# Performance work log

Measured on AMD Instinct MI355X. Metric: run time of the kernel, lower is better.

## Reference

```python
import jax, jax.numpy as jnp
import numpy as np

N = 50000      # nodes
E = 800000     # edges (before self loops)
IN, H, OUT = 128, 64, 64
NEG_SLOPE = 0.2  # PyG GATConv leaky_relu slope


def _glorot(k, shape):
    lim = float(np.sqrt(6.0 / (shape[0] + shape[1])))
    return jax.random.uniform(k, shape, jnp.float32, -lim, lim)


def setup_inputs() -> dict:
    key = jax.random.key(0)
    ks = jax.random.split(key, 16)
    x = jax.random.normal(ks[0], (N, IN), jnp.float32)
    edge_src = jax.random.randint(ks[1], (E,), 0, N, jnp.int32)
    edge_dst = jax.random.randint(ks[2], (E,), 0, N, jnp.int32)
    dims = [(IN, H), (H, H), (H, OUT)]
    inp = {"x": x, "edge_src": edge_src, "edge_dst": edge_dst}
    i = 3
    for l, (di, do) in enumerate(dims):
        inp[f"W{l}"] = _glorot(ks[i], (di, do)); i += 1
        inp[f"as{l}"] = _glorot(ks[i], (1, do))[0]; i += 1
        inp[f"ad{l}"] = _glorot(ks[i], (1, do))[0]; i += 1
        inp[f"b{l}"] = jnp.zeros((do,), jnp.float32)
    return inp


def _gat_layer(x, W, a_src, a_dst, b, src, dst):
    # single-head GATConv (PyG semantics, self loops already in src/dst)
    h = x @ W                              # [N, do]
    s = h @ a_src                          # [N] source attention logits
    d = h @ a_dst                          # [N] dest attention logits
    e = jax.nn.leaky_relu(s[src] + d[dst], NEG_SLOPE)   # [E']
    # segment softmax over incoming edges of each destination node
    m = jax.ops.segment_max(e, dst, num_segments=N)
    w = jnp.exp(e - m[dst])
    denom = jax.ops.segment_sum(w, dst, num_segments=N)
    coef = w / (denom[dst] + 1e-16)
    out = jax.ops.segment_sum(h[src] * coef[:, None], dst, num_segments=N)
    return out + b


def reference(x, edge_src, edge_dst, W0, as0, ad0, b0, W1, as1, ad1, b1, W2, as2, ad2, b2):
    # add self loops (GATConv default add_self_loops=True)
    loop = jnp.arange(N, dtype=edge_src.dtype)
    src = jnp.concatenate([edge_src, loop])
    dst = jnp.concatenate([edge_dst, loop])
    h = jax.nn.relu(_gat_layer(x, W0, as0, ad0, b0, src, dst))
    # dropout is identity in eval mode
    h = jax.nn.relu(_gat_layer(h, W1, as1, ad1, b1, src, dst))
    return _gat_layer(h, W2, as2, ad2, b2, src, dst)
```

## Files before the change

### kernel.cpp

```cpp
#include <hip/hip_runtime.h>
#include <hip/hip_fp16.h>
#include <math.h>

#define WAVE 64
#define NEG_SLOPE 0.2f
#define LSTR 68


__global__ __launch_bounds__(256) void bucket_count_kernel(
    const int* __restrict__ dst, int* __restrict__ gcnt, int e, int nb) {
    extern __shared__ int cnt[];
    for (int b = threadIdx.x; b < nb; b += 256) cnt[b] = 0;
    __syncthreads();
    int base = blockIdx.x * 4096;
#pragma unroll
    for (int k = 0; k < 16; ++k) {
        int i = base + k * 256 + threadIdx.x;
        if (i < e) atomicAdd(&cnt[dst[i] >> 7], 1);
    }
    __syncthreads();
    for (int b = threadIdx.x; b < nb; b += 256) {
        int c = cnt[b];
        if (c) atomicAdd(&gcnt[b], c);
    }
}

__global__ __launch_bounds__(512) void bucket_scan_kernel(
    const int* __restrict__ gcnt, int* __restrict__ boff, int* __restrict__ gfill,
    int* __restrict__ rowptr, int nb, int e, int n) {
    __shared__ int sh[512];
    int t = threadIdx.x;
    int v = (t < nb) ? gcnt[t] : 0;
    sh[t] = v;
    __syncthreads();
    for (int o = 1; o < 512; o <<= 1) {
        int u = (t >= o) ? sh[t - o] : 0;
        __syncthreads();
        sh[t] += u;
        __syncthreads();
    }
    if (t < nb) { int ex = sh[t] - v; boff[t] = ex; gfill[t] = ex; }
    if (t == 0) { boff[nb] = e; rowptr[n] = e + n; }
}

__global__ __launch_bounds__(256) void bucket_place_kernel(
    const int* __restrict__ src, const int* __restrict__ dst,
    int* __restrict__ gfill, int2* __restrict__ binned, int e, int nb) {
    extern __shared__ int lds[];
    int* cnt = lds;
    int* bas = lds + nb;
    for (int b = threadIdx.x; b < nb; b += 256) cnt[b] = 0;
    __syncthreads();
    int base = blockIdx.x * 4096;
#pragma unroll
    for (int k = 0; k < 16; ++k) {
        int i = base + k * 256 + threadIdx.x;
        if (i < e) atomicAdd(&cnt[dst[i] >> 7], 1);
    }
    __syncthreads();
    for (int b = threadIdx.x; b < nb; b += 256) {
        int c = cnt[b];
        bas[b] = c ? atomicAdd(&gfill[b], c) : 0;
        cnt[b] = 0;
    }
    __syncthreads();
#pragma unroll
    for (int k = 0; k < 16; ++k) {
        int i = base + k * 256 + threadIdx.x;
        if (i < e) {
            int d = dst[i];
            int bk = d >> 7;
            int r = atomicAdd(&cnt[bk], 1);
            binned[bas[bk] + r] = make_int2(src[i], d);
        }
    }
}

__global__ __launch_bounds__(256) void bucket_build_kernel(
    const int2* __restrict__ binned, const int* __restrict__ boff,
    int* __restrict__ csr_src, int* __restrict__ rowptr, int n) {
    __shared__ int cnt[128], off[128], pcnt[128];
    int b = blockIdx.x;
    int t = threadIdx.x;
    int nodeBase = b << 7;
    int nc = min(128, n - nodeBase);
    int e0 = boff[b], e1 = boff[b + 1];
    int ne = e1 - e0;
    if (t < 128) { cnt[t] = 1; pcnt[t] = 1; }
    __syncthreads();
    for (int i = t; i < ne; i += 256)
        atomicAdd(&cnt[binned[e0 + i].y - nodeBase], 1);
    __syncthreads();
    if (t < 128) off[t] = cnt[t];
    __syncthreads();
    for (int o = 1; o < 128; o <<= 1) {
        int u = (t >= o && t < 128) ? off[t - o] : 0;
        __syncthreads();
        if (t < 128) off[t] += u;
        __syncthreads();
    }
    if (t < 128) off[t] -= cnt[t];
    __syncthreads();
    int csrBase = e0 + nodeBase;
    if (t < nc) {
        rowptr[nodeBase + t] = csrBase + off[t];
        csr_src[csrBase + off[t]] = nodeBase + t;
    }
    for (int i = t; i < ne; i += 256) {
        int2 p = binned[e0 + i];
        int loc = p.y - nodeBase;
        int r = atomicAdd(&pcnt[loc], 1);
        csr_src[csrBase + off[loc] + r] = p.x;
    }
}


template <int K>
__global__ __launch_bounds__(256) void gemm_feat_kernel(
    const float* __restrict__ X, const float* __restrict__ W,
    const float* __restrict__ a_s, const float* __restrict__ a_d,
    __half* __restrict__ H, float* __restrict__ S, float* __restrict__ D, int n) {
    __shared__ float Xs[64 * LSTR];
    __shared__ float Ws[64 * LSTR];
    int t = threadIdx.x;
    int tx = t & 15;
    int ty = t >> 4;
    int base = blockIdx.x * 64;
    float acc[4][4] = {};

    int q = t & 3;
    int srow = t >> 2;

    for (int k0 = 0; k0 < K; k0 += 64) {
        int grow = base + srow;
#pragma unroll
        for (int j = 0; j < 4; ++j) {
            int c = 16 * j + 4 * q;
            float4 v = make_float4(0.f, 0.f, 0.f, 0.f);
            if (grow < n) v = *(const float4*)(X + (size_t)grow * K + k0 + c);
            *(float4*)(Xs + srow * LSTR + c) = v;
            float4 w = *(const float4*)(W + (size_t)(k0 + srow) * 64 + c);
            *(float4*)(Ws + srow * LSTR + c) = w;
        }
        __syncthreads();
#pragma unroll 8
        for (int kk = 0; kk < 64; ++kk) {
            float4 wv = *(const float4*)(Ws + kk * LSTR + 4 * tx);
#pragma unroll
            for (int i = 0; i < 4; ++i) {
                float xv = Xs[(4 * ty + i) * LSTR + kk];
                acc[i][0] = fmaf(xv, wv.x, acc[i][0]);
                acc[i][1] = fmaf(xv, wv.y, acc[i][1]);
                acc[i][2] = fmaf(xv, wv.z, acc[i][2]);
                acc[i][3] = fmaf(xv, wv.w, acc[i][3]);
            }
        }
        __syncthreads();
    }

    const float4 av_s = *(const float4*)(a_s + 4 * tx);
    const float4 av_d = *(const float4*)(a_d + 4 * tx);
#pragma unroll
    for (int i = 0; i < 4; ++i) {
        int row = base + 4 * ty + i;
        bool ok = row < n;
        if (ok) {
            __half2 h01 = __floats2half2_rn(acc[i][0], acc[i][1]);
            __half2 h23 = __floats2half2_rn(acc[i][2], acc[i][3]);
            uint2 u;
            u.x = *(unsigned int*)&h01;
            u.y = *(unsigned int*)&h23;
            *(uint2*)(H + (size_t)row * 64 + 4 * tx) = u;
        }
        float ps = acc[i][0] * av_s.x + acc[i][1] * av_s.y +
                   acc[i][2] * av_s.z + acc[i][3] * av_s.w;
        float pd = acc[i][0] * av_d.x + acc[i][1] * av_d.y +
                   acc[i][2] * av_d.z + acc[i][3] * av_d.w;
        for (int o = 1; o < 16; o <<= 1) {
            ps += __shfl_xor(ps, o);
            pd += __shfl_xor(pd, o);
        }
        if (tx == 0 && ok) { S[row] = ps; D[row] = pd; }
    }
}


__global__ __launch_bounds__(256) void gat_aggregate_kernel(
    const __half* __restrict__ H, const float* __restrict__ S,
    const float* __restrict__ D, const int* __restrict__ rowptr,
    const int* __restrict__ csr_src, const float* __restrict__ bias,
    float* __restrict__ OUT, int n, int do_relu) {
    int wid  = (blockIdx.x * blockDim.x + threadIdx.x) >> 6;
    int lane = threadIdx.x & 63;
    if (wid >= n) return;
    int eg = lane >> 4;
    int cg = lane & 15;
    int start = rowptr[wid];
    int end   = rowptr[wid + 1];
    float d_i = D[wid];

    float z = 0.f;
    float4 acc = make_float4(0.f, 0.f, 0.f, 0.f);

    for (int cb = start; cb < end; cb += WAVE) {
        int j = cb + lane;
        bool v = j < end;
        int sc = v ? csr_src[j] : 0;
        float sv = S[sc];
        float e = sv + d_i;
        e = (e > 0.f) ? e : NEG_SLOPE * e;
        float w = v ? __expf(e) : 0.f;

        int nch = min(WAVE, end - cb);
        int rounds = (nch + 3) >> 2;
#pragma unroll 4
        for (int r = 0; r < rounds; ++r) {
            int idx = 4 * r + eg;
            float wr = __shfl(w, idx);
            int   sr = __shfl(sc, idx);
            float2 f0 = make_float2(0.f, 0.f), f1 = f0;
            if (idx < nch) {
                uint2 u = *(const uint2*)(H + (size_t)sr * 64 + 4 * cg);
                f0 = __half22float2(*(__half2*)&u.x);
                f1 = __half22float2(*(__half2*)&u.y);
            }
            z += wr;
            acc.x = fmaf(wr, f0.x, acc.x);
            acc.y = fmaf(wr, f0.y, acc.y);
            acc.z = fmaf(wr, f1.x, acc.z);
            acc.w = fmaf(wr, f1.y, acc.w);
        }
    }

    for (int o = 16; o < 64; o <<= 1) {
        acc.x += __shfl_xor(acc.x, o);
        acc.y += __shfl_xor(acc.y, o);
        acc.z += __shfl_xor(acc.z, o);
        acc.w += __shfl_xor(acc.w, o);
        z     += __shfl_xor(z, o);
    }

    if (eg == 0) {
        float inv = 1.f / (z + 1e-16f);
        const float4 bv = *(const float4*)(bias + 4 * cg);
        float4 o4;
        o4.x = acc.x * inv + bv.x;
        o4.y = acc.y * inv + bv.y;
        o4.z = acc.z * inv + bv.z;
        o4.w = acc.w * inv + bv.w;
        if (do_relu) {
            o4.x = fmaxf(o4.x, 0.f); o4.y = fmaxf(o4.y, 0.f);
            o4.z = fmaxf(o4.z, 0.f); o4.w = fmaxf(o4.w, 0.f);
        }
        *(float4*)(OUT + (size_t)wid * 64 + 4 * cg) = o4;
    }
}


static inline size_t align256(size_t x) { return (x + 255) & ~(size_t)255; }

extern "C" void kernel_launch(void* const* d_in, const int* in_sizes, int n_in,
                              void* d_out, int out_size, void* d_ws, size_t ws_size,
                              hipStream_t stream) {
    const float* x    = (const float*)d_in[0];
    const int*   esrc = (const int*)d_in[1];
    const int*   edst = (const int*)d_in[2];
    const int E = in_sizes[1];
    const int N = in_sizes[0] / 128;

    const float* W0 = (const float*)d_in[3];
    const float* as0 = (const float*)d_in[4];
    const float* ad0 = (const float*)d_in[5];
    const float* b0 = (const float*)d_in[6];
    const float* W1 = (const float*)d_in[7];
    const float* as1 = (const float*)d_in[8];
    const float* ad1 = (const float*)d_in[9];
    const float* b1 = (const float*)d_in[10];
    const float* W2 = (const float*)d_in[11];
    const float* as2 = (const float*)d_in[12];
    const float* ad2 = (const float*)d_in[13];
    const float* b2 = (const float*)d_in[14];

    const int NB = (N + 127) >> 7;

    char* p = (char*)d_ws;
    int* gcnt    = (int*)p; p += align256((size_t)(NB + 1) * 4);
    int* boff    = (int*)p; p += align256((size_t)(NB + 1) * 4);
    int* gfill   = (int*)p; p += align256((size_t)(NB + 1) * 4);
    int* rowptr  = (int*)p; p += align256((size_t)(N + 1) * 4);
    int* csr_src = (int*)p; p += align256((size_t)(E + N) * 4);
    int2* binned = (int2*)p; p += align256((size_t)E * 8);
    __half* h16 = (__half*)p; p += align256((size_t)N * 64 * 2);
    float* sA = (float*)p; p += align256((size_t)N * 4);
    float* dA = (float*)p; p += align256((size_t)N * 4);
    float* XA = (float*)p; p += align256((size_t)N * 64 * 4);
    float* XB = (float*)p; p += align256((size_t)N * 64 * 4);
    float* out = (float*)d_out;

    int nchunk = (E + 4095) / 4096;
    hipMemsetAsync(gcnt, 0, (size_t)(NB + 1) * 4, stream);
    bucket_count_kernel<<<nchunk, 256, NB * 4, stream>>>(edst, gcnt, E, NB);
    bucket_scan_kernel<<<1, 512, 0, stream>>>(gcnt, boff, gfill, rowptr, NB, E, N);
    bucket_place_kernel<<<nchunk, 256, 2 * NB * 4, stream>>>(esrc, edst, gfill, binned, E, NB);
    bucket_build_kernel<<<NB, 256, 0, stream>>>(binned, boff, csr_src, rowptr, N);

    int tile_grid = (N + 63) / 64;
    int agg_grid  = (N + 3) / 4;

    gemm_feat_kernel<128><<<tile_grid, 256, 0, stream>>>(x, W0, as0, ad0, h16, sA, dA, N);
    gat_aggregate_kernel<<<agg_grid, 256, 0, stream>>>(h16, sA, dA, rowptr, csr_src, b0, XA, N, 1);

    gemm_feat_kernel<64><<<tile_grid, 256, 0, stream>>>(XA, W1, as1, ad1, h16, sA, dA, N);
    gat_aggregate_kernel<<<agg_grid, 256, 0, stream>>>(h16, sA, dA, rowptr, csr_src, b1, XB, N, 1);

    gemm_feat_kernel<64><<<tile_grid, 256, 0, stream>>>(XB, W2, as2, ad2, h16, sA, dA, N);
    gat_aggregate_kernel<<<agg_grid, 256, 0, stream>>>(h16, sA, dA, rowptr, csr_src, b2, out, N, 0);
}
```

Measured before the change: 272.3 us.

## Fuse aggregation with next-layer GEMM and merge edge counting into layer-0 GEMM

Layer-0 GEMM blocks and edge-count blocks now share one launch, with per-chunk partial counts written to memory instead of global atomics. A column scan in the scan kernel assigns deterministic per-chunk offsets, which removes the memset and the gfill atomics. Aggregation for layers 0 and 1 is fused with the following layer's feature GEMM in 1024-thread blocks, so the fp32 intermediate activations never go to global memory. The cost is a serial per-bucket loop over chunks in the single-block scan, and lower parallelism in the fused kernel, which reads W from global memory rather than LDS.

```diff
diff --git a/kernel.cpp b/kernel.cpp
--- a/kernel.cpp
+++ b/kernel.cpp
@@ -5,129 +5,39 @@
 #define WAVE 64
 #define NEG_SLOPE 0.2f
 #define LSTR 68
-
-
-__global__ __launch_bounds__(256) void bucket_count_kernel(
-    const int* __restrict__ dst, int* __restrict__ gcnt, int e, int nb) {
-    extern __shared__ int cnt[];
-    for (int b = threadIdx.x; b < nb; b += 256) cnt[b] = 0;
-    __syncthreads();
-    int base = blockIdx.x * 4096;
-#pragma unroll
-    for (int k = 0; k < 16; ++k) {
-        int i = base + k * 256 + threadIdx.x;
-        if (i < e) atomicAdd(&cnt[dst[i] >> 7], 1);
-    }
-    __syncthreads();
-    for (int b = threadIdx.x; b < nb; b += 256) {
-        int c = cnt[b];
-        if (c) atomicAdd(&gcnt[b], c);
-    }
-}
-
-__global__ __launch_bounds__(512) void bucket_scan_kernel(
-    const int* __restrict__ gcnt, int* __restrict__ boff, int* __restrict__ gfill,
-    int* __restrict__ rowptr, int nb, int e, int n) {
-    __shared__ int sh[512];
-    int t = threadIdx.x;
-    int v = (t < nb) ? gcnt[t] : 0;
-    sh[t] = v;
-    __syncthreads();
-    for (int o = 1; o < 512; o <<= 1) {
-        int u = (t >= o) ? sh[t - o] : 0;
-        __syncthreads();
-        sh[t] += u;
-        __syncthreads();
-    }
-    if (t < nb) { int ex = sh[t] - v; boff[t] = ex; gfill[t] = ex; }
-    if (t == 0) { boff[nb] = e; rowptr[n] = e + n; }
-}
-
-__global__ __launch_bounds__(256) void bucket_place_kernel(
-    const int* __restrict__ src, const int* __restrict__ dst,
-    int* __restrict__ gfill, int2* __restrict__ binned, int e, int nb) {
-    extern __shared__ int lds[];
-    int* cnt = lds;
-    int* bas = lds + nb;
-    for (int b = threadIdx.x; b < nb; b += 256) cnt[b] = 0;
-    __syncthreads();
-    int base = blockIdx.x * 4096;
-#pragma unroll
-    for (int k = 0; k < 16; ++k) {
-        int i = base + k * 256 + threadIdx.x;
-        if (i < e) atomicAdd(&cnt[dst[i] >> 7], 1);
-    }
-    __syncthreads();
-    for (int b = threadIdx.x; b < nb; b += 256) {
-        int c = cnt[b];
-        bas[b] = c ? atomicAdd(&gfill[b], c) : 0;
-        cnt[b] = 0;
-    }
-    __syncthreads();
-#pragma unroll
-    for (int k = 0; k < 16; ++k) {
-        int i = base + k * 256 + threadIdx.x;
-        if (i < e) {
-            int d = dst[i];
-            int bk = d >> 7;
-            int r = atomicAdd(&cnt[bk], 1);
-            binned[bas[bk] + r] = make_int2(src[i], d);
-        }
-    }
-}
-
-__global__ __launch_bounds__(256) void bucket_build_kernel(
-    const int2* __restrict__ binned, const int* __restrict__ boff,
-    int* __restrict__ csr_src, int* __restrict__ rowptr, int n) {
-    __shared__ int cnt[128], off[128], pcnt[128];
-    int b = blockIdx.x;
-    int t = threadIdx.x;
-    int nodeBase = b << 7;
-    int nc = min(128, n - nodeBase);
-    int e0 = boff[b], e1 = boff[b + 1];
-    int ne = e1 - e0;
-    if (t < 128) { cnt[t] = 1; pcnt[t] = 1; }
-    __syncthreads();
-    for (int i = t; i < ne; i += 256)
-        atomicAdd(&cnt[binned[e0 + i].y - nodeBase], 1);
-    __syncthreads();
-    if (t < 128) off[t] = cnt[t];
-    __syncthreads();
-    for (int o = 1; o < 128; o <<= 1) {
-        int u = (t >= o && t < 128) ? off[t - o] : 0;
-        __syncthreads();
-        if (t < 128) off[t] += u;
-        __syncthreads();
-    }
-    if (t < 128) off[t] -= cnt[t];
-    __syncthreads();
-    int csrBase = e0 + nodeBase;
-    if (t < nc) {
-        rowptr[nodeBase + t] = csrBase + off[t];
-        csr_src[csrBase + off[t]] = nodeBase + t;
-    }
-    for (int i = t; i < ne; i += 256) {
-        int2 p = binned[e0 + i];
-        int loc = p.y - nodeBase;
-        int r = atomicAdd(&pcnt[loc], 1);
-        csr_src[csrBase + off[loc] + r] = p.x;
-    }
-}
-
-
-template <int K>
-__global__ __launch_bounds__(256) void gemm_feat_kernel(
+#define CHUNK 8192
+
+
+__global__ __launch_bounds__(256) void count_gemm0_kernel(
+    const int* __restrict__ dst, int* __restrict__ part, int e, int nb, int nchunk,
     const float* __restrict__ X, const float* __restrict__ W,
     const float* __restrict__ a_s, const float* __restrict__ a_d,
     __half* __restrict__ H, float* __restrict__ S, float* __restrict__ D, int n) {
     __shared__ float Xs[64 * LSTR];
     __shared__ float Ws[64 * LSTR];
     int t = threadIdx.x;
+
+    if (blockIdx.x < nchunk) {
+        int* cnt = (int*)Ws;
+        for (int b = t; b < nb; b += 256) cnt[b] = 0;
+        __syncthreads();
+        int base = blockIdx.x * CHUNK;
+#pragma unroll
+        for (int k = 0; k < CHUNK / 256; ++k) {
+            int i = base + k * 256 + t;
+            if (i < e) atomicAdd(&cnt[dst[i] >> 7], 1);
+        }
+        __syncthreads();
+        for (int b = t; b < nb; b += 256)
+            part[(size_t)blockIdx.x * nb + b] = cnt[b];
+        return;
+    }
+
+    constexpr int K = 128;
     int tx = t & 15;
     int ty = t >> 4;
-    int base = blockIdx.x * 64;
+    int base = (blockIdx.x - nchunk) * 64;
     float acc[4][4] = {};
-
     int q = t & 3;
     int srow = t >> 2;
 
@@ -184,15 +94,111 @@
     }
 }
 
-
-__global__ __launch_bounds__(256) void gat_aggregate_kernel(
+__global__ __launch_bounds__(512) void bucket_scan_kernel(
+    int* __restrict__ part, int* __restrict__ boff, int* __restrict__ rowptr,
+    int nchunk, int nb, int e, int n) {
+    __shared__ int sh[512];
+    int t = threadIdx.x;
+    int total = 0;
+    if (t < nb) {
+        int run = 0;
+        for (int c = 0; c < nchunk; ++c) {
+            size_t idx = (size_t)c * nb + t;
+            int v = part[idx];
+            part[idx] = run;
+            run += v;
+        }
+        total = run;
+    }
+    sh[t] = total;
+    __syncthreads();
+    for (int o = 1; o < 512; o <<= 1) {
+        int u = (t >= o) ? sh[t - o] : 0;
+        __syncthreads();
+        sh[t] += u;
+        __syncthreads();
+    }
+    if (t < nb) boff[t] = sh[t] - total;
+    if (t == 0) { boff[nb] = e; rowptr[n] = e + n; }
+}
+
+__global__ __launch_bounds__(256) void bucket_place_kernel(
+    const int* __restrict__ src, const int* __restrict__ dst,
+    const int* __restrict__ part, const int* __restrict__ boff,
+    int2* __restrict__ binned, int e, int nb) {
+    extern __shared__ int lds[];
+    int* cnt = lds;
+    int* bas = lds + nb;
+    int t = threadIdx.x;
+    for (int b = t; b < nb; b += 256) cnt[b] = 0;
+    __syncthreads();
+    int base = blockIdx.x * CHUNK;
+#pragma unroll
+    for (int k = 0; k < CHUNK / 256; ++k) {
+        int i = base + k * 256 + t;
+        if (i < e) atomicAdd(&cnt[dst[i] >> 7], 1);
+    }
+    __syncthreads();
+    for (int b = t; b < nb; b += 256) {
+        bas[b] = boff[b] + part[(size_t)blockIdx.x * nb + b];
+        cnt[b] = 0;
+    }
+    __syncthreads();
+#pragma unroll
+    for (int k = 0; k < CHUNK / 256; ++k) {
+        int i = base + k * 256 + t;
+        if (i < e) {
+            int d = dst[i];
+            int bk = d >> 7;
+            int r = atomicAdd(&cnt[bk], 1);
+            binned[bas[bk] + r] = make_int2(src[i], d);
+        }
+    }
+}
+
+__global__ __launch_bounds__(256) void bucket_build_kernel(
+    const int2* __restrict__ binned, const int* __restrict__ boff,
+    int* __restrict__ csr_src, int* __restrict__ rowptr, int n) {
+    __shared__ int cnt[128], off[128], pcnt[128];
+    int b = blockIdx.x;
+    int t = threadIdx.x;
+    int nodeBase = b << 7;
+    int nc = min(128, n - nodeBase);
+    int e0 = boff[b], e1 = boff[b + 1];
+    int ne = e1 - e0;
+    if (t < 128) { cnt[t] = 1; pcnt[t] = 1; }
+    __syncthreads();
+    for (int i = t; i < ne; i += 256)
+        atomicAdd(&cnt[binned[e0 + i].y - nodeBase], 1);
+    __syncthreads();
+    if (t < 128) off[t] = cnt[t];
+    __syncthreads();
+    for (int o = 1; o < 128; o <<= 1) {
+        int u = (t >= o && t < 128) ? off[t - o] : 0;
+        __syncthreads();
+        if (t < 128) off[t] += u;
+        __syncthreads();
+    }
+    if (t < 128) off[t] -= cnt[t];
+    __syncthreads();
+    int csrBase = e0 + nodeBase;
+    if (t < nc) {
+        rowptr[nodeBase + t] = csrBase + off[t];
+        csr_src[csrBase + off[t]] = nodeBase + t;
+    }
+    for (int i = t; i < ne; i += 256) {
+        int2 p = binned[e0 + i];
+        int loc = p.y - nodeBase;
+        int r = atomicAdd(&pcnt[loc], 1);
+        csr_src[csrBase + off[loc] + r] = p.x;
+    }
+}
+
+__device__ __forceinline__ float4 gat_node16(
     const __half* __restrict__ H, const float* __restrict__ S,
-    const float* __restrict__ D, const int* __restrict__ rowptr,
-    const int* __restrict__ csr_src, const float* __restrict__ bias,
-    float* __restrict__ OUT, int n, int do_relu) {
-    int wid  = (blockIdx.x * blockDim.x + threadIdx.x) >> 6;
-    int lane = threadIdx.x & 63;
-    if (wid >= n) return;
+    const int* __restrict__ rowptr, const int* __restrict__ csr_src,
+    const float* __restrict__ D, const float4 bv, int wid, int lane,
+    int do_relu) {
     int eg = lane >> 4;
     int cg = lane & 15;
     int start = rowptr[wid];
@@ -240,20 +246,95 @@
         z     += __shfl_xor(z, o);
     }
 
-    if (eg == 0) {
-        float inv = 1.f / (z + 1e-16f);
-        const float4 bv = *(const float4*)(bias + 4 * cg);
-        float4 o4;
-        o4.x = acc.x * inv + bv.x;
-        o4.y = acc.y * inv + bv.y;
-        o4.z = acc.z * inv + bv.z;
-        o4.w = acc.w * inv + bv.w;
-        if (do_relu) {
-            o4.x = fmaxf(o4.x, 0.f); o4.y = fmaxf(o4.y, 0.f);
-            o4.z = fmaxf(o4.z, 0.f); o4.w = fmaxf(o4.w, 0.f);
-        }
-        *(float4*)(OUT + (size_t)wid * 64 + 4 * cg) = o4;
-    }
+    float inv = 1.f / (z + 1e-16f);
+    float4 o4;
+    o4.x = acc.x * inv + bv.x;
+    o4.y = acc.y * inv + bv.y;
+    o4.z = acc.z * inv + bv.z;
+    o4.w = acc.w * inv + bv.w;
+    if (do_relu) {
+        o4.x = fmaxf(o4.x, 0.f); o4.y = fmaxf(o4.y, 0.f);
+        o4.z = fmaxf(o4.z, 0.f); o4.w = fmaxf(o4.w, 0.f);
+    }
+    return o4;
+}
+
+__global__ __launch_bounds__(1024, 8) void agg_gemm_kernel(
+    const __half* __restrict__ Hin, const float* __restrict__ Sin,
+    const float* __restrict__ Din, const int* __restrict__ rowptr,
+    const int* __restrict__ csr_src, const float* __restrict__ bias,
+    const float* __restrict__ W, const float* __restrict__ a_s,
+    const float* __restrict__ a_d, __half* __restrict__ Hout,
+    float* __restrict__ Sout, float* __restrict__ Dout, int n) {
+    __shared__ float Xs[64 * LSTR];
+    int t = threadIdx.x;
+    int lane = t & 63;
+    int wv = t >> 6;
+    int base = blockIdx.x * 64;
+    int eg = lane >> 4;
+    int cg = lane & 15;
+    const float4 bv = *(const float4*)(bias + 4 * cg);
+
+#pragma unroll
+    for (int k = 0; k < 4; ++k) {
+        int local = 4 * wv + k;
+        int wid = base + local;
+        if (wid < n) {
+            float4 o4 = gat_node16(Hin, Sin, rowptr, csr_src, Din, bv, wid, lane, 1);
+            if (eg == 0) *(float4*)(Xs + local * LSTR + 4 * cg) = o4;
+        } else if (eg == 0) {
+            *(float4*)(Xs + local * LSTR + 4 * cg) = make_float4(0.f, 0.f, 0.f, 0.f);
+        }
+    }
+    __syncthreads();
+
+    int row = t >> 4;
+    int txq = t & 15;
+    float a0 = 0.f, a1 = 0.f, a2 = 0.f, a3 = 0.f;
+#pragma unroll 8
+    for (int kk = 0; kk < 64; ++kk) {
+        float xv = Xs[row * LSTR + kk];
+        float4 wv4 = *(const float4*)(W + kk * 64 + 4 * txq);
+        a0 = fmaf(xv, wv4.x, a0);
+        a1 = fmaf(xv, wv4.y, a1);
+        a2 = fmaf(xv, wv4.z, a2);
+        a3 = fmaf(xv, wv4.w, a3);
+    }
+
+    int grow = base + row;
+    bool ok = grow < n;
+    if (ok) {
+        __half2 h01 = __floats2half2_rn(a0, a1);
+        __half2 h23 = __floats2half2_rn(a2, a3);
+        uint2 u;
+        u.x = *(unsigned int*)&h01;
+        u.y = *(unsigned int*)&h23;
+        *(uint2*)(Hout + (size_t)grow * 64 + 4 * txq) = u;
+    }
+    const float4 av_s = *(const float4*)(a_s + 4 * txq);
+    const float4 av_d = *(const float4*)(a_d + 4 * txq);
+    float ps = a0 * av_s.x + a1 * av_s.y + a2 * av_s.z + a3 * av_s.w;
+    float pd = a0 * av_d.x + a1 * av_d.y + a2 * av_d.z + a3 * av_d.w;
+    for (int o = 1; o < 16; o <<= 1) {
+        ps += __shfl_xor(ps, o);
+        pd += __shfl_xor(pd, o);
+    }
+    if (txq == 0 && ok) { Sout[grow] = ps; Dout[grow] = pd; }
+}
+
+__global__ __launch_bounds__(256) void gat_aggregate_kernel(
+    const __half* __restrict__ H, const float* __restrict__ S,
+    const float* __restrict__ D, const int* __restrict__ rowptr,
+    const int* __restrict__ csr_src, const float* __restrict__ bias,
+    float* __restrict__ OUT, int n) {
+    int wid  = (blockIdx.x * blockDim.x + threadIdx.x) >> 6;
+    int lane = threadIdx.x & 63;
+    if (wid >= n) return;
+    int eg = lane >> 4;
+    int cg = lane & 15;
+    const float4 bv = *(const float4*)(bias + 4 * cg);
+    float4 o4 = gat_node16(H, S, rowptr, csr_src, D, bv, wid, lane, 0);
+    if (eg == 0) *(float4*)(OUT + (size_t)wid * 64 + 4 * cg) = o4;
 }
 
 
@@ -282,37 +363,33 @@
     const float* b2 = (const float*)d_in[14];
 
     const int NB = (N + 127) >> 7;
+    const int nchunk = (E + CHUNK - 1) / CHUNK;
 
     char* p = (char*)d_ws;
-    int* gcnt    = (int*)p; p += align256((size_t)(NB + 1) * 4);
+    int* part    = (int*)p; p += align256((size_t)nchunk * NB * 4);
     int* boff    = (int*)p; p += align256((size_t)(NB + 1) * 4);
-    int* gfill   = (int*)p; p += align256((size_t)(NB + 1) * 4);
     int* rowptr  = (int*)p; p += align256((size_t)(N + 1) * 4);
     int* csr_src = (int*)p; p += align256((size_t)(E + N) * 4);
     int2* binned = (int2*)p; p += align256((size_t)E * 8);
-    __half* h16 = (__half*)p; p += align256((size_t)N * 64 * 2);
+    __half* hA = (__half*)p; p += align256((size_t)N * 64 * 2);
+    __half* hB = (__half*)p; p += align256((size_t)N * 64 * 2);
     float* sA = (float*)p; p += align256((size_t)N * 4);
     float* dA = (float*)p; p += align256((size_t)N * 4);
-    float* XA = (float*)p; p += align256((size_t)N * 64 * 4);
-    float* XB = (float*)p; p += align256((size_t)N * 64 * 4);
+    float* sB = (float*)p; p += align256((size_t)N * 4);
+    float* dB = (float*)p; p += align256((size_t)N * 4);
     float* out = (float*)d_out;
-
-    int nchunk = (E + 4095) / 4096;
-    hipMemsetAsync(gcnt, 0, (size_t)(NB + 1) * 4, stream);
-    bucket_count_kernel<<<nchunk, 256, NB * 4, stream>>>(edst, gcnt, E, NB);
-    bucket_scan_kernel<<<1, 512, 0, stream>>>(gcnt, boff, gfill, rowptr, NB, E, N);
-    bucket_place_kernel<<<nchunk, 256, 2 * NB * 4, stream>>>(esrc, edst, gfill, binned, E, NB);
-    bucket_build_kernel<<<NB, 256, 0, stream>>>(binned, boff, csr_src, rowptr, N);
 
     int tile_grid = (N + 63) / 64;
     int agg_grid  = (N + 3) / 4;
 
-    gemm_feat_kernel<128><<<tile_grid, 256, 0, stream>>>(x, W0, as0, ad0, h16, sA, dA, N);
-    gat_aggregate_kernel<<<agg_grid, 256, 0, stream>>>(h16, sA, dA, rowptr, csr_src, b0, XA, N, 1);
-
-    gemm_feat_kernel<64><<<tile_grid, 256, 0, stream>>>(XA, W1, as1, ad1, h16, sA, dA, N);
-    gat_aggregate_kernel<<<agg_grid, 256, 0, stream>>>(h16, sA, dA, rowptr, csr_src, b1, XB, N, 1);
-
-    gemm_feat_kernel<64><<<tile_grid, 256, 0, stream>>>(XB, W2, as2, ad2, h16, sA, dA, N);
-    gat_aggregate_kernel<<<agg_grid, 256, 0, stream>>>(h16, sA, dA, rowptr, csr_src, b2, out, N, 0);
-}
+    count_gemm0_kernel<<<nchunk + tile_grid, 256, 0, stream>>>(
+        edst, part, E, NB, nchunk, x, W0, as0, ad0, hA, sA, dA, N);
+    bucket_scan_kernel<<<1, 512, 0, stream>>>(part, boff, rowptr, nchunk, NB, E, N);
+    bucket_place_kernel<<<nchunk, 256, 2 * NB * 4, stream>>>(esrc, edst, part, boff, binned, E, NB);
+    bucket_build_kernel<<<NB, 256, 0, stream>>>(binned, boff, csr_src, rowptr, N);
+    agg_gemm_kernel<<<tile_grid, 1024, 0, stream>>>(hA, sA, dA, rowptr, csr_src, b0,
+                                                    W1, as1, ad1, hB, sB, dB, N);
+    agg_gemm_kernel<<<tile_grid, 1024, 0, stream>>>(hB, sB, dB, rowptr, csr_src, b1,
+                                                    W2, as2, ad2, hA, sA, dA, N);
+    gat_aggregate_kernel<<<agg_grid, 256, 0, stream>>>(hA, sA, dA, rowptr, csr_src, b2, out, N);
+}
```

After: 319.4 us. 17.3% more time.
